# Optimization experiments

Measured on AMD Instinct MI355X. Metric: run time of the kernel, lower is better.

## Reference

```python
import jax, jax.numpy as jnp
import numpy as np

BS, SEQ, D_MODEL, N_HEADS = 4, 2048, 1024, 16
D_HEAD = D_MODEL // N_HEADS


def setup_inputs() -> dict:
    key = jax.random.key(0)
    ks = jax.random.split(key, 12)
    s = 1.0 / np.sqrt(D_MODEL)
    return {
        "Q": jax.random.normal(ks[0], (BS, SEQ, D_MODEL), jnp.float32),
        "K": jax.random.normal(ks[1], (BS, SEQ, D_MODEL), jnp.float32),
        "V": jax.random.normal(ks[2], (BS, SEQ, D_MODEL), jnp.float32),
        "mask": jax.random.randint(ks[3], (BS, 1, 1, SEQ), 0, 2, jnp.int32),
        "Wq": jax.random.normal(ks[4], (D_MODEL, D_MODEL), jnp.float32) * s,
        "bq": jnp.zeros((D_MODEL,), jnp.float32),
        "Wk": jax.random.normal(ks[5], (D_MODEL, D_MODEL), jnp.float32) * s,
        "bk": jnp.zeros((D_MODEL,), jnp.float32),
        "Wv": jax.random.normal(ks[6], (D_MODEL, D_MODEL), jnp.float32) * s,
        "bv": jnp.zeros((D_MODEL,), jnp.float32),
        "Wo": jax.random.normal(ks[7], (D_MODEL, D_MODEL), jnp.float32) * s,
        "bo": jnp.zeros((D_MODEL,), jnp.float32),
    }


def _split_heads(x):
    # (b, s, d_model) -> (b, h, s, d_head)
    b, s, _ = x.shape
    return x.reshape(b, s, N_HEADS, D_HEAD).transpose(0, 2, 1, 3)


def reference(Q, K, V, mask, Wq, bq, Wk, bk, Wv, bv, Wo, bo):
    q = _split_heads(Q @ Wq.T + bq)
    k = _split_heads(K @ Wk.T + bk)
    v = _split_heads(V @ Wv.T + bv)
    # (b, h, sq, sk) score matrix, scaled by sqrt(d_head)
    scores = jnp.einsum("bhqd,bhkd->bhqk", q, k) / np.sqrt(D_HEAD).astype(np.float32)
    scores = jnp.where(mask == 0, jnp.float32(-1e9), scores)
    attn = jax.nn.softmax(scores, axis=-1)
    ctx = jnp.einsum("bhqk,bhkd->bhqd", attn, v)
    b, h, s, d = ctx.shape
    ctx = ctx.transpose(0, 2, 1, 3).reshape(b, s, h * d)
    return ctx @ Wo.T + bo
```

## Files before the change

### kernel.cpp

```cpp
#include <hip/hip_runtime.h>


typedef __attribute__((ext_vector_type(8))) unsigned short us8;
typedef __attribute__((ext_vector_type(4))) unsigned short us4;
typedef __attribute__((ext_vector_type(4))) int i4;
typedef __attribute__((ext_vector_type(4))) float f4;
typedef __attribute__((ext_vector_type(4))) float f32x4;
typedef __attribute__((ext_vector_type(8))) __bf16 bf16x8;
typedef __attribute__((ext_vector_type(2))) unsigned u32x2;
typedef __attribute__((ext_vector_type(4))) unsigned u32x4;

#define DEV static __device__ __forceinline__

DEV unsigned short f2bf(float f){
  unsigned u = __builtin_bit_cast(unsigned, f);
  u = (u + 0x7fffu + ((u >> 16) & 1u)) >> 16;
  return (unsigned short)u;
}

DEV bf16x8 ld_frag(const unsigned short* p){
  return __builtin_bit_cast(bf16x8, *(const us8*)p);
}

DEV void gll16(const unsigned short* gsrc, unsigned short* ldst){
  __builtin_amdgcn_global_load_lds(
      (const __attribute__((address_space(1))) unsigned int*)gsrc,
      (__attribute__((address_space(3))) unsigned int*)ldst, 16, 0, 0);
}

DEV us8 ld_cvt_f32x8(const float* p){
  f4 v0 = *(const f4*)p;
  f4 v1 = *(const f4*)(p + 4);
  unsigned d0, d1, d2, d3;
  asm("v_cvt_pk_bf16_f32 %0, %1, %2" : "=v"(d0) : "v"(v0[0]), "v"(v0[1]));
  asm("v_cvt_pk_bf16_f32 %0, %1, %2" : "=v"(d1) : "v"(v0[2]), "v"(v0[3]));
  asm("v_cvt_pk_bf16_f32 %0, %1, %2" : "=v"(d2) : "v"(v1[0]), "v"(v1[1]));
  asm("v_cvt_pk_bf16_f32 %0, %1, %2" : "=v"(d3) : "v"(v1[2]), "v"(v1[3]));
  u32x4 u = {d0, d1, d2, d3};
  return __builtin_bit_cast(us8, u);
}

__global__ void cvt_bf16(const float* __restrict__ in, unsigned short* __restrict__ out, int n8){
  int i = blockIdx.x * 256 + threadIdx.x;
  if(i >= n8) return;
  *(us8*)(out + (size_t)i * 8) = ld_cvt_f32x8(in + (size_t)i * 8);
}

__global__ __launch_bounds__(256) void mask_scan(
    const int* __restrict__ mask, int* __restrict__ idx, int* __restrict__ nk)
{
  const int b = blockIdx.x, t = threadIdx.x;
  __shared__ int sc[256];
  int m[8]; int c = 0;
#pragma unroll
  for(int r = 0; r < 8; ++r){ m[r] = mask[b * 2048 + t * 8 + r]; c += (m[r] != 0); }
  sc[t] = c;
  __syncthreads();
  for(int s = 1; s < 256; s <<= 1){
    int v = (t >= s) ? sc[t - s] : 0;
    __syncthreads();
    sc[t] += v;
    __syncthreads();
  }
  int pos = sc[t] - c;
  int total = sc[255];
#pragma unroll
  for(int r = 0; r < 8; ++r) if(m[r]) idx[b * 2048 + pos++] = t * 8 + r;
  int pend = (total + 127) & ~127;
  for(int p = total + t; p < pend; p += 256) idx[b * 2048 + p] = 0;
  if(t == 0) nk[b] = total;
}

template<int MODE, bool AF32, bool BF32, int GATHER, bool SWAPG>
__global__ __launch_bounds__(256) void gemm_bt(
    const void* __restrict__ Ap, const void* __restrict__ Bp,
    const float* __restrict__ bias, void* __restrict__ outp,
    int M, int N, int K, float scale,
    const int* __restrict__ gidx, const int* __restrict__ nkarr)
{
  __shared__ __align__(16) unsigned short As[128 * 64];
  __shared__ __align__(16) unsigned short Bs[128 * 64];
  const int tid = threadIdx.x;
  const int gx = SWAPG ? blockIdx.y : blockIdx.x;
  const int gy = SWAPG ? blockIdx.x : blockIdx.y;
  const int w = tid >> 6, l = tid & 63, g = l >> 4, l15 = l & 15;
  const int wm = w >> 1, wn = w & 1;
  const int xsw = ((l & 7) ^ (l >> 3)) << 3;
  const int ch = tid & 7, srow = tid >> 3;

  int ia[4];
  int gb = 0;
  if constexpr(GATHER != 0){
    const int tilerow = (GATHER == 1) ? gy : gx;
    gb = (tilerow * 128) >> 11;
    const int j0 = (tilerow * 128) & 2047;
    const int total = nkarr[gb];
    if(j0 >= ((total + 127) & ~127)) return;
#pragma unroll
    for(int i = 0; i < 4; ++i)
      ia[i] = gidx[gb * 2048 + j0 + srow + i * 32];
  }

  f32x4 acc[4][4];
#pragma unroll
  for(int a = 0; a < 4; ++a)
#pragma unroll
    for(int b = 0; b < 4; ++b) acc[a][b] = (f32x4){0.f,0.f,0.f,0.f};

  const int nkt = K >> 6;
  for(int kt = 0; kt < nkt; ++kt){
    __syncthreads();
    if constexpr(AF32){
#pragma unroll
      for(int i = 0; i < 4; ++i){
        int row = srow + i * 32;
        const float* src;
        if constexpr(GATHER == 1)
          src = (const float*)Ap + ((size_t)gb * 2048 + ia[i]) * K + kt * 64 + ch * 8;
        else
          src = (const float*)Ap + (size_t)(gy * 128 + row) * K + kt * 64 + ch * 8;
        us8 va = ld_cvt_f32x8(src);
        *(us8*)&As[row * 64 + ((ch * 8) ^ ((row & 7) << 3))] = va;
      }
    } else {
      const unsigned short* Ab = (const unsigned short*)Ap;
#pragma unroll
      for(int j = 0; j < 4; ++j)
        gll16(Ab + (size_t)(gy * 128 + (w << 5) + (j << 3) + (l >> 3)) * K + kt * 64 + xsw,
              &As[((w << 5) + (j << 3)) << 6]);
    }
    if constexpr(BF32){
#pragma unroll
      for(int i = 0; i < 4; ++i){
        int row = srow + i * 32;
        const float* src;
        if constexpr(GATHER == 2)
          src = (const float*)Bp + ((size_t)gb * 2048 + ia[i]) * K + kt * 64 + ch * 8;
        else
          src = (const float*)Bp + (size_t)(gx * 128 + row) * K + kt * 64 + ch * 8;
        us8 vb = ld_cvt_f32x8(src);
        *(us8*)&Bs[row * 64 + ((ch * 8) ^ ((row & 7) << 3))] = vb;
      }
    } else {
      const unsigned short* Bb = (const unsigned short*)Bp;
#pragma unroll
      for(int j = 0; j < 4; ++j)
        gll16(Bb + (size_t)(gx * 128 + (w << 5) + (j << 3) + (l >> 3)) * K + kt * 64 + xsw,
              &Bs[((w << 5) + (j << 3)) << 6]);
    }
    if constexpr(!(AF32 && BF32))
      asm volatile("s_waitcnt vmcnt(0)" ::: "memory");
    __syncthreads();
#pragma unroll
    for(int kk = 0; kk < 2; ++kk){
      bf16x8 af[4], bg[4];
#pragma unroll
      for(int mi = 0; mi < 4; ++mi){
        int row = wm * 64 + mi * 16 + l15;
        af[mi] = ld_frag(&As[row * 64 + ((kk * 32 + g * 8) ^ ((row & 7) << 3))]);
      }
#pragma unroll
      for(int ni = 0; ni < 4; ++ni){
        int row = wn * 64 + ni * 16 + l15;
        bg[ni] = ld_frag(&Bs[row * 64 + ((kk * 32 + g * 8) ^ ((row & 7) << 3))]);
      }
#pragma unroll
      for(int mi = 0; mi < 4; ++mi)
#pragma unroll
        for(int ni = 0; ni < 4; ++ni)
          acc[mi][ni] = __builtin_amdgcn_mfma_f32_16x16x32_bf16(af[mi], bg[ni], acc[mi][ni], 0, 0, 0);
    }
  }

#pragma unroll
  for(int mi = 0; mi < 4; ++mi)
#pragma unroll
    for(int ni = 0; ni < 4; ++ni){
      int gmb = gy * 128 + wm * 64 + mi * 16 + g * 4;
      int gn  = gx * 128 + wn * 64 + ni * 16 + l15;
#pragma unroll
      for(int r = 0; r < 4; ++r){
        int gm = gmb + r;
        float v = acc[mi][ni][r];
        if(MODE == 0){
          v = (v + bias[gn]) * scale;
          int b = gm >> 11, s = gm & 2047, h = gn >> 6, dh = gn & 63;
          ((unsigned short*)outp)[(size_t)(((b << 4) + h) * 2048 + s) * 64 + dh] = f2bf(v);
        } else if(MODE == 1){
          v = v + bias[gm];
          int h = gm >> 6, dh = gm & 63, b = gn >> 11, s = gn & 2047;
          ((unsigned short*)outp)[(size_t)(((b << 4) + h) * 64 + dh) * 2048 + s] = f2bf(v);
        } else {
          v = v + bias[gn];
          ((float*)outp)[(size_t)gm * N + gn] = v;
        }
      }
    }
}

__global__ __launch_bounds__(256) void attn_kernel(
    const unsigned short* __restrict__ q, const unsigned short* __restrict__ ksc,
    const unsigned short* __restrict__ vTc, const int* __restrict__ nk,
    unsigned short* __restrict__ ctx)
{
  __shared__ __align__(16) unsigned short KsB[2][64 * 64];
  __shared__ __align__(16) unsigned short VtB[2][64 * 64];
  __shared__ __align__(16) unsigned short Ps[4][16 * 64];

  const int qt = blockIdx.x;
  const int bh = blockIdx.y;
  const int b  = bh >> 4, h = bh & 15;
  const int tid = threadIdx.x;
  const int w = tid >> 6, l = tid & 63, g = l >> 4, l15 = l & 15;
  const int rl = l >> 3, c8 = l & 7;

  const int nkb = nk[b];
  const int nt = (nkb + 63) >> 6;

  const unsigned short* qbase = q + ((size_t)(bh * 2048 + qt * 64 + w * 16 + l15)) * 64;
  bf16x8 bq[2];
  bq[0] = ld_frag(qbase + g * 8);
  bq[1] = ld_frag(qbase + 32 + g * 8);

  const unsigned short* kbase = ksc + (size_t)bh * 2048 * 64;
  const unsigned short* vbase = vTc + (size_t)bh * 64 * 2048;

  const unsigned short* kg0 = kbase + (size_t)(w * 16 + rl) * 64 + c8 * 8;
  const unsigned short* vg0 = vbase + (size_t)(w * 16 + rl) * 2048 + c8 * 8;
  const int lo0 = (w * 16 + rl) * 64 + ((c8 ^ rl) << 3);
  const int lo1 = lo0 + 8 * 64;

  us8 kr0, kr1, vr0, vr1;
#define LOAD_T(kt_) do{                                        \
    kr0 = *(const us8*)(kg0 + (size_t)(kt_) * 4096);           \
    kr1 = *(const us8*)(kg0 + (size_t)(kt_) * 4096 + 512);     \
    vr0 = *(const us8*)(vg0 + (size_t)(kt_) * 64);             \
    vr1 = *(const us8*)(vg0 + (size_t)(kt_) * 64 + 8 * 2048);  \
  }while(0)
#define WRITE_T(bb_) do{                                       \
    *(us8*)&KsB[bb_][lo0] = kr0;                               \
    *(us8*)&KsB[bb_][lo1] = kr1;                               \
    *(us8*)&VtB[bb_][lo0] = vr0;                               \
    *(us8*)&VtB[bb_][lo1] = vr1;                               \
  }while(0)

  f32x4 acc[4];
#pragma unroll
  for(int mi = 0; mi < 4; ++mi) acc[mi] = (f32x4){0.f,0.f,0.f,0.f};
  float ll = 0.f;

  LOAD_T(0);
  WRITE_T(0);
  __syncthreads();

  for(int kt = 0; kt < nt; ++kt){
    const int bb = kt & 1;
    if(kt + 1 < nt) LOAD_T(kt + 1);

    f32x4 sa[4];
#pragma unroll
    for(int mi = 0; mi < 4; ++mi) sa[mi] = (f32x4){0.f,0.f,0.f,0.f};
#pragma unroll
    for(int kk = 0; kk < 2; ++kk){
#pragma unroll
      for(int mi = 0; mi < 4; ++mi){
        int row = mi * 16 + l15;
        bf16x8 af = ld_frag(&KsB[bb][row * 64 + ((kk * 32 + g * 8) ^ ((row & 7) << 3))]);
        sa[mi] = __builtin_amdgcn_mfma_f32_16x16x32_bf16(af, bq[kk], sa[mi], 0, 0, 0);
      }
    }

    float p[4][4];
    if((kt + 1) * 64 <= nkb){
#pragma unroll
      for(int mi = 0; mi < 4; ++mi)
#pragma unroll
        for(int r = 0; r < 4; ++r){
          p[mi][r] = __builtin_amdgcn_exp2f(sa[mi][r]);
          ll += p[mi][r];
        }
    } else {
      int kb0 = kt * 64 + g * 4;
#pragma unroll
      for(int mi = 0; mi < 4; ++mi)
#pragma unroll
        for(int r = 0; r < 4; ++r){
          float e = __builtin_amdgcn_exp2f(sa[mi][r]);
          p[mi][r] = (kb0 + mi * 16 + r < nkb) ? e : 0.f;
          ll += p[mi][r];
        }
    }

#pragma unroll
    for(int mi = 0; mi < 4; ++mi){
      unsigned d0, d1;
      asm("v_cvt_pk_bf16_f32 %0, %1, %2" : "=v"(d0) : "v"(p[mi][0]), "v"(p[mi][1]));
      asm("v_cvt_pk_bf16_f32 %0, %1, %2" : "=v"(d1) : "v"(p[mi][2]), "v"(p[mi][3]));
      u32x2 dd = {d0, d1};
      *(u32x2*)&Ps[w][l15 * 64 + ((mi * 16 + g * 4) ^ ((l15 & 7) << 3))] = dd;
    }

#pragma unroll
    for(int kk = 0; kk < 2; ++kk){
      bf16x8 pb = ld_frag(&Ps[w][l15 * 64 + ((kk * 32 + g * 8) ^ ((l15 & 7) << 3))]);
#pragma unroll
      for(int mi = 0; mi < 4; ++mi){
        int row = mi * 16 + l15;
        bf16x8 av = ld_frag(&VtB[bb][row * 64 + ((kk * 32 + g * 8) ^ ((row & 7) << 3))]);
        acc[mi] = __builtin_amdgcn_mfma_f32_16x16x32_bf16(av, pb, acc[mi], 0, 0, 0);
      }
    }

    if(kt + 1 < nt) WRITE_T(bb ^ 1);
    __syncthreads();
  }

  ll += __shfl_xor(ll, 16);
  ll += __shfl_xor(ll, 32);
  float inv = 1.0f / ll;

  {
    int qrow = w * 16 + l15;
#pragma unroll
    for(int mi = 0; mi < 4; ++mi){
      us4 o;
#pragma unroll
      for(int r = 0; r < 4; ++r) o[r] = f2bf(acc[mi][r] * inv);
      *(us4*)&KsB[0][qrow * 64 + ((mi * 16 + g * 4) ^ ((qrow & 7) << 3))] = o;
    }
  }
  __syncthreads();
  {
    int qrow = tid >> 2, part = tid & 3;
    us8 v0 = *(const us8*)&KsB[0][qrow * 64 + ((part * 16)     ^ ((qrow & 7) << 3))];
    us8 v1 = *(const us8*)&KsB[0][qrow * 64 + ((part * 16 + 8) ^ ((qrow & 7) << 3))];
    size_t orow = ((size_t)b * 2048 + qt * 64 + qrow) * 1024 + h * 64 + part * 16;
    *(us8*)&ctx[orow] = v0;
    *(us8*)&ctx[orow + 8] = v1;
  }
#undef LOAD_T
#undef WRITE_T
}

extern "C" void kernel_launch(void* const* d_in, const int* in_sizes, int n_in,
                              void* d_out, int out_size, void* d_ws, size_t ws_size,
                              hipStream_t stream) {
  const float* Qf = (const float*)d_in[0];
  const float* Kf = (const float*)d_in[1];
  const float* Vf = (const float*)d_in[2];
  const int*   Mk = (const int*)d_in[3];
  const float* Wq = (const float*)d_in[4];
  const float* bq = (const float*)d_in[5];
  const float* Wk = (const float*)d_in[6];
  const float* bk = (const float*)d_in[7];
  const float* Wv = (const float*)d_in[8];
  const float* bv = (const float*)d_in[9];
  const float* Wo = (const float*)d_in[10];
  const float* bo = (const float*)d_in[11];

  const size_t MB = 1u << 20;
  char* ws = (char*)d_ws;
  unsigned short* Wqb = (unsigned short*)(ws + 0 * MB);
  unsigned short* Wkb = (unsigned short*)(ws + 2 * MB);
  unsigned short* Wvb = (unsigned short*)(ws + 4 * MB);
  unsigned short* Wob = (unsigned short*)(ws + 6 * MB);
  unsigned short* qs  = (unsigned short*)(ws + 8 * MB);
  unsigned short* ksc = (unsigned short*)(ws + 24 * MB);
  unsigned short* vTc = (unsigned short*)(ws + 40 * MB);
  unsigned short* ctx = (unsigned short*)(ws + 56 * MB);
  int* idx = (int*)(ws + 72 * MB);
  int* nk  = (int*)(ws + 73 * MB);

  const int NW = 1024 * 1024;

  auto cvt = [&](const float* src, unsigned short* dst, int n){
    int n8 = n / 8;
    cvt_bf16<<<(n8 + 255) / 256, 256, 0, stream>>>(src, dst, n8);
  };
  cvt(Wq, Wqb, NW);
  cvt(Wk, Wkb, NW);
  cvt(Wv, Wvb, NW);
  cvt(Wo, Wob, NW);

  mask_scan<<<4, 256, 0, stream>>>(Mk, idx, nk);

  const float QSCALE = 0.125f * 1.4426950408889634f;
  dim3 blk(256);
  gemm_bt<0, true, false, 0, true><<<dim3(64, 8), blk, 0, stream>>>(
      Qf, Wqb, bq, qs, 8192, 1024, 1024, QSCALE, nullptr, nullptr);
  gemm_bt<0, true, false, 1, true><<<dim3(64, 8), blk, 0, stream>>>(
      Kf, Wkb, bk, ksc, 8192, 1024, 1024, 1.0f, idx, nk);
  gemm_bt<1, false, true, 2, false><<<dim3(64, 8), blk, 0, stream>>>(
      Wvb, Vf, bv, vTc, 1024, 8192, 1024, 1.0f, idx, nk);
  attn_kernel<<<dim3(32, 64), blk, 0, stream>>>(qs, ksc, vTc, nk, ctx);
  gemm_bt<2, false, false, 0, true><<<dim3(64, 8), blk, 0, stream>>>(
      ctx, Wob, bo, d_out, 8192, 1024, 1024, 1.0f, nullptr, nullptr);
}
```

Measured before the change: 187.6 us.

## Merge Q/K/V projection GEMMs into one launch and prioritize attention MFMA

Replaces the three separate projection GEMM launches with a single qkv_proj kernel whose grid's y dimension selects Q, K or V, so all 1536 tiles share one launch and can fill the GPU together. The templated GEMM is split into a specialized projection kernel and an output GEMM. The attention kernel raises wave priority around its MFMA sections using s_setprio. mask_scan is moved earlier in the stream. Runtime branching on z adds some divergence and register pressure, and the merged kernel's skipped gather tiles may leave the load uneven.

New measurement: 182.2 us. -2.9%, faster.

```diff
diff --git a/kernel.cpp b/kernel.cpp
--- a/kernel.cpp
+++ b/kernel.cpp
@@ -71,18 +71,19 @@
   if(t == 0) nk[b] = total;
 }
 
-template<int MODE, bool AF32, bool BF32, int GATHER, bool SWAPG>
-__global__ __launch_bounds__(256) void gemm_bt(
-    const void* __restrict__ Ap, const void* __restrict__ Bp,
-    const float* __restrict__ bias, void* __restrict__ outp,
-    int M, int N, int K, float scale,
+__global__ __launch_bounds__(256) void qkv_proj(
+    const float* __restrict__ Qf, const float* __restrict__ Kf, const float* __restrict__ Vf,
+    const unsigned short* __restrict__ Wqb, const unsigned short* __restrict__ Wkb,
+    const unsigned short* __restrict__ Wvb,
+    const float* __restrict__ bq, const float* __restrict__ bk, const float* __restrict__ bv,
+    unsigned short* __restrict__ qs, unsigned short* __restrict__ ksc,
+    unsigned short* __restrict__ vTc, float qscale,
     const int* __restrict__ gidx, const int* __restrict__ nkarr)
 {
   __shared__ __align__(16) unsigned short As[128 * 64];
   __shared__ __align__(16) unsigned short Bs[128 * 64];
   const int tid = threadIdx.x;
-  const int gx = SWAPG ? blockIdx.y : blockIdx.x;
-  const int gy = SWAPG ? blockIdx.x : blockIdx.y;
+  const int x = blockIdx.x, z = blockIdx.y >> 3, ny = blockIdx.y & 7;
   const int w = tid >> 6, l = tid & 63, g = l >> 4, l15 = l & 15;
   const int wm = w >> 1, wn = w & 1;
   const int xsw = ((l & 7) ^ (l >> 3)) << 3;
@@ -90,66 +91,54 @@
 
   int ia[4];
   int gb = 0;
-  if constexpr(GATHER != 0){
-    const int tilerow = (GATHER == 1) ? gy : gx;
-    gb = (tilerow * 128) >> 11;
-    const int j0 = (tilerow * 128) & 2047;
-    const int total = nkarr[gb];
-    if(j0 >= ((total + 127) & ~127)) return;
+  if(z >= 1){
+    gb = (x * 128) >> 11;
+    const int j0 = (x * 128) & 2047;
+    if(j0 >= ((nkarr[gb] + 127) & ~127)) return;
 #pragma unroll
     for(int i = 0; i < 4; ++i)
       ia[i] = gidx[gb * 2048 + j0 + srow + i * 32];
   }
 
+  const float*          Af32 = (z == 0) ? Qf : Kf;
+  const unsigned short* Wb   = (z == 0) ? Wqb : Wkb;
+
   f32x4 acc[4][4];
 #pragma unroll
   for(int a = 0; a < 4; ++a)
 #pragma unroll
     for(int b = 0; b < 4; ++b) acc[a][b] = (f32x4){0.f,0.f,0.f,0.f};
 
-  const int nkt = K >> 6;
-  for(int kt = 0; kt < nkt; ++kt){
-    __syncthreads();
-    if constexpr(AF32){
+  for(int kt = 0; kt < 16; ++kt){
+    __syncthreads();
+    if(z < 2){
 #pragma unroll
       for(int i = 0; i < 4; ++i){
         int row = srow + i * 32;
-        const float* src;
-        if constexpr(GATHER == 1)
-          src = (const float*)Ap + ((size_t)gb * 2048 + ia[i]) * K + kt * 64 + ch * 8;
-        else
-          src = (const float*)Ap + (size_t)(gy * 128 + row) * K + kt * 64 + ch * 8;
+        const float* src = (z == 1)
+          ? Af32 + ((size_t)gb * 2048 + ia[i]) * 1024 + kt * 64 + ch * 8
+          : Af32 + (size_t)(x * 128 + row) * 1024 + kt * 64 + ch * 8;
         us8 va = ld_cvt_f32x8(src);
         *(us8*)&As[row * 64 + ((ch * 8) ^ ((row & 7) << 3))] = va;
       }
+#pragma unroll
+      for(int j = 0; j < 4; ++j)
+        gll16(Wb + (size_t)(ny * 128 + (w << 5) + (j << 3) + (l >> 3)) * 1024 + kt * 64 + xsw,
+              &Bs[((w << 5) + (j << 3)) << 6]);
     } else {
-      const unsigned short* Ab = (const unsigned short*)Ap;
 #pragma unroll
       for(int j = 0; j < 4; ++j)
-        gll16(Ab + (size_t)(gy * 128 + (w << 5) + (j << 3) + (l >> 3)) * K + kt * 64 + xsw,
+        gll16(Wvb + (size_t)(ny * 128 + (w << 5) + (j << 3) + (l >> 3)) * 1024 + kt * 64 + xsw,
               &As[((w << 5) + (j << 3)) << 6]);
-    }
-    if constexpr(BF32){
 #pragma unroll
       for(int i = 0; i < 4; ++i){
         int row = srow + i * 32;
-        const float* src;
-        if constexpr(GATHER == 2)
-          src = (const float*)Bp + ((size_t)gb * 2048 + ia[i]) * K + kt * 64 + ch * 8;
-        else
-          src = (const float*)Bp + (size_t)(gx * 128 + row) * K + kt * 64 + ch * 8;
+        const float* src = Vf + ((size_t)gb * 2048 + ia[i]) * 1024 + kt * 64 + ch * 8;
         us8 vb = ld_cvt_f32x8(src);
         *(us8*)&Bs[row * 64 + ((ch * 8) ^ ((row & 7) << 3))] = vb;
       }
-    } else {
-      const unsigned short* Bb = (const unsigned short*)Bp;
-#pragma unroll
-      for(int j = 0; j < 4; ++j)
-        gll16(Bb + (size_t)(gx * 128 + (w << 5) + (j << 3) + (l >> 3)) * K + kt * 64 + xsw,
-              &Bs[((w << 5) + (j << 3)) << 6]);
-    }
-    if constexpr(!(AF32 && BF32))
-      asm volatile("s_waitcnt vmcnt(0)" ::: "memory");
+    }
+    asm volatile("s_waitcnt vmcnt(0)" ::: "memory");
     __syncthreads();
 #pragma unroll
     for(int kk = 0; kk < 2; ++kk){
@@ -172,6 +161,94 @@
     }
   }
 
+  if(z < 2){
+    const float scale = (z == 0) ? qscale : 1.0f;
+    const float* bias = (z == 0) ? bq : bk;
+    unsigned short* out = (z == 0) ? qs : ksc;
+#pragma unroll
+    for(int mi = 0; mi < 4; ++mi)
+#pragma unroll
+      for(int ni = 0; ni < 4; ++ni){
+        int gmb = x * 128 + wm * 64 + mi * 16 + g * 4;
+        int gn  = ny * 128 + wn * 64 + ni * 16 + l15;
+#pragma unroll
+        for(int r = 0; r < 4; ++r){
+          int gm = gmb + r;
+          float v = (acc[mi][ni][r] + bias[gn]) * scale;
+          int b = gm >> 11, s = gm & 2047, h = gn >> 6, dh = gn & 63;
+          out[(size_t)(((b << 4) + h) * 2048 + s) * 64 + dh] = f2bf(v);
+        }
+      }
+  } else {
+#pragma unroll
+    for(int mi = 0; mi < 4; ++mi)
+#pragma unroll
+      for(int ni = 0; ni < 4; ++ni){
+        int gmb = ny * 128 + wm * 64 + mi * 16 + g * 4;
+        int gn  = x * 128 + wn * 64 + ni * 16 + l15;
+#pragma unroll
+        for(int r = 0; r < 4; ++r){
+          int gm = gmb + r;
+          float v = acc[mi][ni][r] + bv[gm];
+          int h = gm >> 6, dh = gm & 63, b = gn >> 11, s = gn & 2047;
+          vTc[(size_t)(((b << 4) + h) * 64 + dh) * 2048 + s] = f2bf(v);
+        }
+      }
+  }
+}
+
+__global__ __launch_bounds__(256) void gemm_out(
+    const unsigned short* __restrict__ Ap, const unsigned short* __restrict__ Bp,
+    const float* __restrict__ bias, float* __restrict__ outp, int K)
+{
+  __shared__ __align__(16) unsigned short As[128 * 64];
+  __shared__ __align__(16) unsigned short Bs[128 * 64];
+  const int tid = threadIdx.x;
+  const int gy = blockIdx.x, gx = blockIdx.y;
+  const int w = tid >> 6, l = tid & 63, g = l >> 4, l15 = l & 15;
+  const int wm = w >> 1, wn = w & 1;
+  const int xsw = ((l & 7) ^ (l >> 3)) << 3;
+
+  f32x4 acc[4][4];
+#pragma unroll
+  for(int a = 0; a < 4; ++a)
+#pragma unroll
+    for(int b = 0; b < 4; ++b) acc[a][b] = (f32x4){0.f,0.f,0.f,0.f};
+
+  const int nkt = K >> 6;
+  for(int kt = 0; kt < nkt; ++kt){
+    __syncthreads();
+#pragma unroll
+    for(int j = 0; j < 4; ++j)
+      gll16(Ap + (size_t)(gy * 128 + (w << 5) + (j << 3) + (l >> 3)) * K + kt * 64 + xsw,
+            &As[((w << 5) + (j << 3)) << 6]);
+#pragma unroll
+    for(int j = 0; j < 4; ++j)
+      gll16(Bp + (size_t)(gx * 128 + (w << 5) + (j << 3) + (l >> 3)) * K + kt * 64 + xsw,
+            &Bs[((w << 5) + (j << 3)) << 6]);
+    asm volatile("s_waitcnt vmcnt(0)" ::: "memory");
+    __syncthreads();
+#pragma unroll
+    for(int kk = 0; kk < 2; ++kk){
+      bf16x8 af[4], bg[4];
+#pragma unroll
+      for(int mi = 0; mi < 4; ++mi){
+        int row = wm * 64 + mi * 16 + l15;
+        af[mi] = ld_frag(&As[row * 64 + ((kk * 32 + g * 8) ^ ((row & 7) << 3))]);
+      }
+#pragma unroll
+      for(int ni = 0; ni < 4; ++ni){
+        int row = wn * 64 + ni * 16 + l15;
+        bg[ni] = ld_frag(&Bs[row * 64 + ((kk * 32 + g * 8) ^ ((row & 7) << 3))]);
+      }
+#pragma unroll
+      for(int mi = 0; mi < 4; ++mi)
+#pragma unroll
+        for(int ni = 0; ni < 4; ++ni)
+          acc[mi][ni] = __builtin_amdgcn_mfma_f32_16x16x32_bf16(af[mi], bg[ni], acc[mi][ni], 0, 0, 0);
+    }
+  }
+
 #pragma unroll
   for(int mi = 0; mi < 4; ++mi)
 #pragma unroll
@@ -179,22 +256,8 @@
       int gmb = gy * 128 + wm * 64 + mi * 16 + g * 4;
       int gn  = gx * 128 + wn * 64 + ni * 16 + l15;
 #pragma unroll
-      for(int r = 0; r < 4; ++r){
-        int gm = gmb + r;
-        float v = acc[mi][ni][r];
-        if(MODE == 0){
-          v = (v + bias[gn]) * scale;
-          int b = gm >> 11, s = gm & 2047, h = gn >> 6, dh = gn & 63;
-          ((unsigned short*)outp)[(size_t)(((b << 4) + h) * 2048 + s) * 64 + dh] = f2bf(v);
-        } else if(MODE == 1){
-          v = v + bias[gm];
-          int h = gm >> 6, dh = gm & 63, b = gn >> 11, s = gn & 2047;
-          ((unsigned short*)outp)[(size_t)(((b << 4) + h) * 64 + dh) * 2048 + s] = f2bf(v);
-        } else {
-          v = v + bias[gn];
-          ((float*)outp)[(size_t)gm * N + gn] = v;
-        }
-      }
+      for(int r = 0; r < 4; ++r)
+        outp[(size_t)(gmb + r) * 1024 + gn] = acc[mi][ni][r] + bias[gn];
     }
 }
 
@@ -260,6 +323,7 @@
     f32x4 sa[4];
 #pragma unroll
     for(int mi = 0; mi < 4; ++mi) sa[mi] = (f32x4){0.f,0.f,0.f,0.f};
+    __builtin_amdgcn_s_setprio(1);
 #pragma unroll
     for(int kk = 0; kk < 2; ++kk){
 #pragma unroll
@@ -269,6 +333,7 @@
         sa[mi] = __builtin_amdgcn_mfma_f32_16x16x32_bf16(af, bq[kk], sa[mi], 0, 0, 0);
       }
     }
+    __builtin_amdgcn_s_setprio(0);
 
     float p[4][4];
     if((kt + 1) * 64 <= nkb){
@@ -300,6 +365,7 @@
       *(u32x2*)&Ps[w][l15 * 64 + ((mi * 16 + g * 4) ^ ((l15 & 7) << 3))] = dd;
     }
 
+    __builtin_amdgcn_s_setprio(1);
 #pragma unroll
     for(int kk = 0; kk < 2; ++kk){
       bf16x8 pb = ld_frag(&Ps[w][l15 * 64 + ((kk * 32 + g * 8) ^ ((l15 & 7) << 3))]);
@@ -310,6 +376,7 @@
         acc[mi] = __builtin_amdgcn_mfma_f32_16x16x32_bf16(av, pb, acc[mi], 0, 0, 0);
       }
     }
+    __builtin_amdgcn_s_setprio(0);
 
     if(kt + 1 < nt) WRITE_T(bb ^ 1);
     __syncthreads();
@@ -373,6 +440,8 @@
 
   const int NW = 1024 * 1024;
 
+  mask_scan<<<4, 256, 0, stream>>>(Mk, idx, nk);
+
   auto cvt = [&](const float* src, unsigned short* dst, int n){
     int n8 = n / 8;
     cvt_bf16<<<(n8 + 255) / 256, 256, 0, stream>>>(src, dst, n8);
@@ -382,17 +451,11 @@
   cvt(Wv, Wvb, NW);
   cvt(Wo, Wob, NW);
 
-  mask_scan<<<4, 256, 0, stream>>>(Mk, idx, nk);
-
   const float QSCALE = 0.125f * 1.4426950408889634f;
   dim3 blk(256);
-  gemm_bt<0, true, false, 0, true><<<dim3(64, 8), blk, 0, stream>>>(
-      Qf, Wqb, bq, qs, 8192, 1024, 1024, QSCALE, nullptr, nullptr);
-  gemm_bt<0, true, false, 1, true><<<dim3(64, 8), blk, 0, stream>>>(
-      Kf, Wkb, bk, ksc, 8192, 1024, 1024, 1.0f, idx, nk);
-  gemm_bt<1, false, true, 2, false><<<dim3(64, 8), blk, 0, stream>>>(
-      Wvb, Vf, bv, vTc, 1024, 8192, 1024, 1.0f, idx, nk);
+  qkv_proj<<<dim3(64, 24), blk, 0, stream>>>(Qf, Kf, Vf, Wqb, Wkb, Wvb,
+                                             bq, bk, bv, qs, ksc, vTc, QSCALE,
+                                             idx, nk);
   attn_kernel<<<dim3(32, 64), blk, 0, stream>>>(qs, ksc, vTc, nk, ctx);
-  gemm_bt<2, false, false, 0, true><<<dim3(64, 8), blk, 0, stream>>>(
-      ctx, Wob, bo, d_out, 8192, 1024, 1024, 1.0f, nullptr, nullptr);
-}
+  gemm_out<<<dim3(64, 8), blk, 0, stream>>>(ctx, Wob, bo, (float*)d_out, 1024);
+}
```
